# Kernel optimization log

Measured on AMD Instinct MI355X. Metric: run time of the kernel, lower is better.

## Reference

```python
import jax, jax.numpy as jnp
import numpy as np

B, DEC, ENC, H = 4, 128, 512, 768


def setup_inputs() -> dict:
    key = jax.random.key(0)
    k1, k2, k3, k4, k5 = jax.random.split(key, 5)
    scale = 1.0 / np.sqrt(H)
    return {
        "decoder_state": jax.random.normal(k1, (B, DEC, H), dtype=jnp.float32),
        "encoder_outputs": jax.random.normal(k2, (B, ENC, H), dtype=jnp.float32),
        "mask": jnp.zeros((B, DEC, ENC), dtype=jnp.float32),
        # Learned params: torch nn.Linear(H, H, bias=False) weights, stored as (in, out)
        "W1": jax.random.normal(k3, (H, H), dtype=jnp.float32) * scale,
        "W2": jax.random.normal(k4, (H, H), dtype=jnp.float32) * scale,
        "vt": jax.random.normal(k5, (H,), dtype=jnp.float32) * scale,
    }


def reference(decoder_state, encoder_outputs, mask, W1, W2, vt):
    # enc_t: (B, enc, H), dec_t: (B, dec, H)
    enc_t = jnp.einsum("beh,hk->bek", encoder_outputs, W1)
    dec_t = jnp.einsum("bdh,hk->bdk", decoder_state, W2)
    # Bahdanau additive score: tanh of broadcast sum -> (B, dec, enc, H), reduce with vt
    hidden = jnp.tanh(enc_t[:, None, :, :] + dec_t[:, :, None, :])
    log_score = jnp.einsum("bdek,k->bde", hidden, vt)
    log_score_masked = log_score + mask
    return (log_score_masked, log_score)
```

## Files before the change

### kernel.cpp

```cpp
#include <hip/hip_runtime.h>
#include <hip/hip_bf16.h>

#define B_SZ   4
#define DEC_SZ 128
#define ENC_SZ 512
#define H_SZ   768

typedef __attribute__((ext_vector_type(8))) short s8v;
typedef __attribute__((ext_vector_type(4))) float fvec4;

__device__ inline unsigned short f2bf(float x) {
  union { float f; unsigned u; } v; v.f = x;
  unsigned r = v.u + 0x7FFF + ((v.u >> 16) & 1);
  return (unsigned short)(r >> 16);
}

__global__ __launch_bounds__(256) void transpose_w(const float* __restrict__ W1,
                                                   const float* __restrict__ W2,
                                                   unsigned short* __restrict__ T1,
                                                   unsigned short* __restrict__ T2) {
  const float* W = blockIdx.z ? W2 : W1;
  unsigned short* T = blockIdx.z ? T2 : T1;
  __shared__ float tile[64][65];
  int c0 = blockIdx.x * 64;
  int r0 = blockIdx.y * 64;
  int tx = threadIdx.x & 63, ty = threadIdx.x >> 6;
#pragma unroll
  for (int i = 0; i < 16; ++i) {
    int r = ty + i * 4;
    tile[r][tx] = W[(size_t)(r0 + r) * H_SZ + c0 + tx];
  }
  __syncthreads();
#pragma unroll
  for (int i = 0; i < 16; ++i) {
    int c = ty + i * 4;
    T[(size_t)(c0 + c) * H_SZ + r0 + tx] = f2bf(tile[tx][c]);
  }
}

__global__ __launch_bounds__(256) void cast_bf16(const float* __restrict__ x,
                                                 unsigned short* __restrict__ y, int n4) {
  int i = blockIdx.x * 256 + threadIdx.x;
  if (i >= n4) return;
  float4 v = ((const float4*)x)[i];
  ushort4 o;
  o.x = f2bf(v.x); o.y = f2bf(v.y); o.z = f2bf(v.z); o.w = f2bf(v.w);
  ((ushort4*)y)[i] = o;
}

__global__ __launch_bounds__(256) void gemm_nt_exp(const unsigned short* __restrict__ A,
                                                   size_t strideA,
                                                   const unsigned short* __restrict__ Bm,
                                                   size_t strideB,
                                                   float* __restrict__ C, size_t strideC,
                                                   int ldc) {
  const int b  = blockIdx.z;
  const int m0 = blockIdx.x * 128;
  const int n0 = blockIdx.y * 128;
  const unsigned short* Ab = A + strideA * (size_t)b;
  const unsigned short* Bb = Bm + strideB * (size_t)b;

  __shared__ unsigned short As[128][40];
  __shared__ unsigned short Bs[128][40];

  const int tid  = threadIdx.x;
  const int wave = tid >> 6;
  const int lane = tid & 63;
  const int l16  = lane & 15;
  const int quad = lane >> 4;
  const int wm = (wave & 1) * 64;
  const int wn = (wave >> 1) * 64;

  fvec4 acc[4][4];
#pragma unroll
  for (int i = 0; i < 4; ++i)
#pragma unroll
    for (int j = 0; j < 4; ++j) acc[i][j] = (fvec4)0.f;

  for (int k0 = 0; k0 < H_SZ; k0 += 32) {
#pragma unroll
    for (int i = 0; i < 2; ++i) {
      int seg = tid + 256 * i;
      int r = seg >> 2, k8 = (seg & 3) * 8;
      *(s8v*)&As[r][k8] = *(const s8v*)(Ab + (size_t)(m0 + r) * H_SZ + k0 + k8);
      *(s8v*)&Bs[r][k8] = *(const s8v*)(Bb + (size_t)(n0 + r) * H_SZ + k0 + k8);
    }
    __syncthreads();

    s8v af[4], bf[4];
#pragma unroll
    for (int i = 0; i < 4; ++i) af[i] = *(const s8v*)&As[wm + i * 16 + l16][quad * 8];
#pragma unroll
    for (int j = 0; j < 4; ++j) bf[j] = *(const s8v*)&Bs[wn + j * 16 + l16][quad * 8];
#pragma unroll
    for (int i = 0; i < 4; ++i)
#pragma unroll
      for (int j = 0; j < 4; ++j)
        acc[i][j] = __builtin_amdgcn_mfma_f32_16x16x32_bf16(af[i], bf[j], acc[i][j], 0, 0, 0);
    __syncthreads();
  }

  const float C2 = 2.885390082f;
  float* Cb = C + strideC * (size_t)b;
#pragma unroll
  for (int i = 0; i < 4; ++i) {
    int m = m0 + wm + i * 16 + quad * 4;
#pragma unroll
    for (int j = 0; j < 4; ++j) {
      int n = n0 + wn + j * 16 + l16;
#pragma unroll
      for (int r = 0; r < 4; ++r)
        Cb[(size_t)(m + r) * ldc + n] = exp2f(acc[i][j][r] * C2);
    }
  }
}

#define D_CHUNK 8
#define K_CHUNK 96
#define NKC     8

__global__ __launch_bounds__(256) void score_kernel(const float* __restrict__ peT,
                                                    const float* __restrict__ pdm,
                                                    const float* __restrict__ vt,
                                                    float* __restrict__ part) {
  const int e  = blockIdx.x * 256 + threadIdx.x;
  const int d0 = blockIdx.y * D_CHUNK;
  const int bz = blockIdx.z;
  const int b  = bz >> 3;
  const int kc = bz & 7;
  const int k0 = kc * K_CHUNK;
  const int tid = threadIdx.x;

  __shared__ float pd_s[K_CHUNK][D_CHUNK];
  __shared__ float vts[K_CHUNK];

#pragma unroll
  for (int i = 0; i < 3; ++i) {
    int idx = tid + 256 * i;
    int d = idx / K_CHUNK, k = idx % K_CHUNK;
    pd_s[k][d] = pdm[((size_t)b * DEC_SZ + d0 + d) * H_SZ + k0 + k];
  }
  if (tid < K_CHUNK) vts[tid] = vt[k0 + tid];
  __syncthreads();

  float sumv = 0.f;
  for (int k = 0; k < K_CHUNK; ++k) sumv += vts[k];

  float t[D_CHUNK];
#pragma unroll
  for (int d = 0; d < D_CHUNK; ++d) t[d] = 0.f;

  const float* ep = peT + ((size_t)b * H_SZ + k0) * ENC_SZ + e;

#pragma unroll 4
  for (int k = 0; k < K_CHUNK; ++k) {
    float pe = ep[(size_t)k * ENC_SZ];
    float vk = vts[k];
    const float4 p0 = *(const float4*)&pd_s[k][0];
    const float4 p1 = *(const float4*)&pd_s[k][4];
    float pd[8] = {p0.x, p0.y, p0.z, p0.w, p1.x, p1.y, p1.z, p1.w};
#pragma unroll
    for (int d = 0; d < D_CHUNK; ++d) {
      float r = __builtin_amdgcn_rcpf(fmaf(pe, pd[d], 1.f));
      t[d] = fmaf(vk, r, t[d]);
    }
  }

  float* pp = part + (size_t)kc * (B_SZ * DEC_SZ * ENC_SZ) +
              ((size_t)b * DEC_SZ + d0) * ENC_SZ + e;
#pragma unroll
  for (int d = 0; d < D_CHUNK; ++d)
    pp[(size_t)d * ENC_SZ] = fmaf(-2.f, t[d], sumv);
}

__global__ __launch_bounds__(256) void finalize_kernel(const float* __restrict__ part,
                                                       const float* __restrict__ mask,
                                                       float* __restrict__ out) {
  const int N  = B_SZ * DEC_SZ * ENC_SZ;
  const int N4 = N / 4;
  int i = blockIdx.x * 256 + threadIdx.x;
  if (i >= N4) return;
  const float4* p = (const float4*)part;
  float4 s = p[i];
#pragma unroll
  for (int kc = 1; kc < NKC; ++kc) {
    float4 q = p[i + kc * N4];
    s.x += q.x; s.y += q.y; s.z += q.z; s.w += q.w;
  }
  float4 m = ((const float4*)mask)[i];
  float4 sm;
  sm.x = s.x + m.x; sm.y = s.y + m.y; sm.z = s.z + m.z; sm.w = s.w + m.w;
  ((float4*)out)[i] = sm;
  ((float4*)(out + N))[i] = s;
}

extern "C" void kernel_launch(void* const* d_in, const int* in_sizes, int n_in,
                              void* d_out, int out_size, void* d_ws, size_t ws_size,
                              hipStream_t stream) {
  (void)in_sizes; (void)n_in; (void)out_size; (void)ws_size;
  const float* dec  = (const float*)d_in[0];
  const float* enc  = (const float*)d_in[1];
  const float* mask = (const float*)d_in[2];
  const float* W1   = (const float*)d_in[3];
  const float* W2   = (const float*)d_in[4];
  const float* vt   = (const float*)d_in[5];
  float* out = (float*)d_out;

  float* peT  = (float*)d_ws;
  float* pdm  = peT + (size_t)B_SZ * H_SZ * ENC_SZ;
  float* part = pdm + (size_t)B_SZ * DEC_SZ * H_SZ;
  unsigned short* W1T  = (unsigned short*)(part + (size_t)NKC * B_SZ * DEC_SZ * ENC_SZ);
  unsigned short* W2T  = W1T + (size_t)H_SZ * H_SZ;
  unsigned short* encB = W2T + (size_t)H_SZ * H_SZ;
  unsigned short* decB = encB + (size_t)B_SZ * ENC_SZ * H_SZ;

  transpose_w<<<dim3(12, 12, 2), 256, 0, stream>>>(W1, W2, W1T, W2T);
  cast_bf16<<<dim3((B_SZ * ENC_SZ * H_SZ / 4 + 255) / 256), 256, 0, stream>>>(
      enc, encB, B_SZ * ENC_SZ * H_SZ / 4);
  cast_bf16<<<dim3((B_SZ * DEC_SZ * H_SZ / 4 + 255) / 256), 256, 0, stream>>>(
      dec, decB, B_SZ * DEC_SZ * H_SZ / 4);

  gemm_nt_exp<<<dim3(H_SZ / 128, ENC_SZ / 128, B_SZ), 256, 0, stream>>>(
      W1T, 0, encB, (size_t)ENC_SZ * H_SZ, peT, (size_t)H_SZ * ENC_SZ, ENC_SZ);
  gemm_nt_exp<<<dim3(DEC_SZ / 128, H_SZ / 128, B_SZ), 256, 0, stream>>>(
      decB, (size_t)DEC_SZ * H_SZ, W2T, 0, pdm, (size_t)DEC_SZ * H_SZ, H_SZ);

  score_kernel<<<dim3(ENC_SZ / 256, DEC_SZ / D_CHUNK, B_SZ * NKC), 256, 0, stream>>>(
      peT, pdm, vt, part);
  finalize_kernel<<<dim3(B_SZ * DEC_SZ * ENC_SZ / 4 / 256), 256, 0, stream>>>(
      part, mask, out);
}
```

Before: 145.7 us.

## Fuse score reduction with finalize, retile GEMMs with register prefetch, merge casts

Drops the split-K score kernel, its partial buffer and the separate finalize pass. A single score_out kernel now loops over all of H per (e, d) tile and writes both outputs with the mask added directly. The GEMMs switch to smaller templated tiles (TM x 64) with register prefetch of the next K slice, and batches fold into the M/N dimension. The two cast launches merge into one, and exp2f becomes the hardware builtin. This removes the partial-sum traffic and two launches, at the cost of less parallelism per score block (128 threads, full-K serial loop).

```diff
diff --git a/kernel.cpp b/kernel.cpp
--- a/kernel.cpp
+++ b/kernel.cpp
@@ -5,6 +5,7 @@
 #define DEC_SZ 128
 #define ENC_SZ 512
 #define H_SZ   768
+#define OUT_N  (B_SZ * DEC_SZ * ENC_SZ)
 
 typedef __attribute__((ext_vector_type(8))) short s8v;
 typedef __attribute__((ext_vector_type(4))) float fvec4;
@@ -38,8 +39,13 @@
   }
 }
 
-__global__ __launch_bounds__(256) void cast_bf16(const float* __restrict__ x,
-                                                 unsigned short* __restrict__ y, int n4) {
+__global__ __launch_bounds__(256) void cast_bf16(const float* __restrict__ enc,
+                                                 const float* __restrict__ dec,
+                                                 unsigned short* __restrict__ encB,
+                                                 unsigned short* __restrict__ decB) {
+  const float* x = blockIdx.z ? dec : enc;
+  unsigned short* y = blockIdx.z ? decB : encB;
+  int n4 = blockIdx.z ? (B_SZ * DEC_SZ * H_SZ / 4) : (B_SZ * ENC_SZ * H_SZ / 4);
   int i = blockIdx.x * 256 + threadIdx.x;
   if (i >= n4) return;
   float4 v = ((const float4*)x)[i];
@@ -48,150 +54,157 @@
   ((ushort4*)y)[i] = o;
 }
 
+template <int TM>
 __global__ __launch_bounds__(256) void gemm_nt_exp(const unsigned short* __restrict__ A,
-                                                   size_t strideA,
                                                    const unsigned short* __restrict__ Bm,
-                                                   size_t strideB,
-                                                   float* __restrict__ C, size_t strideC,
-                                                   int ldc) {
-  const int b  = blockIdx.z;
-  const int m0 = blockIdx.x * 128;
-  const int n0 = blockIdx.y * 128;
-  const unsigned short* Ab = A + strideA * (size_t)b;
-  const unsigned short* Bb = Bm + strideB * (size_t)b;
-
-  __shared__ unsigned short As[128][40];
-  __shared__ unsigned short Bs[128][40];
+                                                   float* __restrict__ C, int ldc) {
+  const int m0 = blockIdx.x * TM;
+  const int n0 = blockIdx.y * 64;
+
+  __shared__ unsigned short As[TM][40];
+  __shared__ unsigned short Bs[64][40];
 
   const int tid  = threadIdx.x;
   const int wave = tid >> 6;
   const int lane = tid & 63;
   const int l16  = lane & 15;
   const int quad = lane >> 4;
-  const int wm = (wave & 1) * 64;
-  const int wn = (wave >> 1) * 64;
-
-  fvec4 acc[4][4];
-#pragma unroll
-  for (int i = 0; i < 4; ++i)
+  const int MI   = TM / 64;
+  const int wm   = wave * (TM / 4);
+
+  const int ASEG = TM * 4 / 256;
+  int ar[2], ak[2];
+#pragma unroll
+  for (int i = 0; i < ASEG; ++i) {
+    int seg = tid + 256 * i;
+    ar[i] = seg >> 2; ak[i] = (seg & 3) * 8;
+  }
+  const int br = tid >> 2, bk = (tid & 3) * 8;
+
+  fvec4 acc[2][4];
+#pragma unroll
+  for (int i = 0; i < 2; ++i)
 #pragma unroll
     for (int j = 0; j < 4; ++j) acc[i][j] = (fvec4)0.f;
 
+  s8v pa[2], pb;
+#pragma unroll
+  for (int i = 0; i < ASEG; ++i)
+    pa[i] = *(const s8v*)(A + (size_t)(m0 + ar[i]) * H_SZ + ak[i]);
+  pb = *(const s8v*)(Bm + (size_t)(n0 + br) * H_SZ + bk);
+
   for (int k0 = 0; k0 < H_SZ; k0 += 32) {
-#pragma unroll
-    for (int i = 0; i < 2; ++i) {
-      int seg = tid + 256 * i;
-      int r = seg >> 2, k8 = (seg & 3) * 8;
-      *(s8v*)&As[r][k8] = *(const s8v*)(Ab + (size_t)(m0 + r) * H_SZ + k0 + k8);
-      *(s8v*)&Bs[r][k8] = *(const s8v*)(Bb + (size_t)(n0 + r) * H_SZ + k0 + k8);
-    }
     __syncthreads();
-
-    s8v af[4], bf[4];
-#pragma unroll
-    for (int i = 0; i < 4; ++i) af[i] = *(const s8v*)&As[wm + i * 16 + l16][quad * 8];
-#pragma unroll
-    for (int j = 0; j < 4; ++j) bf[j] = *(const s8v*)&Bs[wn + j * 16 + l16][quad * 8];
-#pragma unroll
-    for (int i = 0; i < 4; ++i)
+#pragma unroll
+    for (int i = 0; i < ASEG; ++i) *(s8v*)&As[ar[i]][ak[i]] = pa[i];
+    *(s8v*)&Bs[br][bk] = pb;
+    __syncthreads();
+
+    if (k0 + 32 < H_SZ) {
+#pragma unroll
+      for (int i = 0; i < ASEG; ++i)
+        pa[i] = *(const s8v*)(A + (size_t)(m0 + ar[i]) * H_SZ + k0 + 32 + ak[i]);
+      pb = *(const s8v*)(Bm + (size_t)(n0 + br) * H_SZ + k0 + 32 + bk);
+    }
+
+    s8v af[2], bf[4];
+#pragma unroll
+    for (int i = 0; i < MI; ++i) af[i] = *(const s8v*)&As[wm + i * 16 + l16][quad * 8];
+#pragma unroll
+    for (int j = 0; j < 4; ++j) bf[j] = *(const s8v*)&Bs[j * 16 + l16][quad * 8];
+#pragma unroll
+    for (int i = 0; i < MI; ++i)
 #pragma unroll
       for (int j = 0; j < 4; ++j)
         acc[i][j] = __builtin_amdgcn_mfma_f32_16x16x32_bf16(af[i], bf[j], acc[i][j], 0, 0, 0);
-    __syncthreads();
   }
 
   const float C2 = 2.885390082f;
-  float* Cb = C + strideC * (size_t)b;
-#pragma unroll
-  for (int i = 0; i < 4; ++i) {
+#pragma unroll
+  for (int i = 0; i < MI; ++i) {
     int m = m0 + wm + i * 16 + quad * 4;
 #pragma unroll
     for (int j = 0; j < 4; ++j) {
-      int n = n0 + wn + j * 16 + l16;
+      int n = n0 + j * 16 + l16;
 #pragma unroll
       for (int r = 0; r < 4; ++r)
-        Cb[(size_t)(m + r) * ldc + n] = exp2f(acc[i][j][r] * C2);
-    }
-  }
-}
-
-#define D_CHUNK 8
-#define K_CHUNK 96
-#define NKC     8
-
-__global__ __launch_bounds__(256) void score_kernel(const float* __restrict__ peT,
-                                                    const float* __restrict__ pdm,
-                                                    const float* __restrict__ vt,
-                                                    float* __restrict__ part) {
-  const int e  = blockIdx.x * 256 + threadIdx.x;
-  const int d0 = blockIdx.y * D_CHUNK;
-  const int bz = blockIdx.z;
-  const int b  = bz >> 3;
-  const int kc = bz & 7;
-  const int k0 = kc * K_CHUNK;
-  const int tid = threadIdx.x;
-
-  __shared__ float pd_s[K_CHUNK][D_CHUNK];
-  __shared__ float vts[K_CHUNK];
-
-#pragma unroll
-  for (int i = 0; i < 3; ++i) {
-    int idx = tid + 256 * i;
-    int d = idx / K_CHUNK, k = idx % K_CHUNK;
-    pd_s[k][d] = pdm[((size_t)b * DEC_SZ + d0 + d) * H_SZ + k0 + k];
-  }
-  if (tid < K_CHUNK) vts[tid] = vt[k0 + tid];
+        C[(size_t)(m + r) * ldc + n] = __builtin_amdgcn_exp2f(acc[i][j][r] * C2);
+    }
+  }
+}
+
+__global__ __launch_bounds__(128) void score_out(const float* __restrict__ peT,
+                                                 const float* __restrict__ pdm,
+                                                 const float* __restrict__ vt,
+                                                 const float* __restrict__ mask,
+                                                 float* __restrict__ out) {
+  const int tid  = threadIdx.x;
+  const int wave = tid >> 6;
+  const int lane = tid & 63;
+  const int e    = blockIdx.x * 64 + lane;
+  const int d0   = blockIdx.y * 8;
+  const int b    = blockIdx.z;
+
+  __shared__ float pd_s[H_SZ][8];
+  __shared__ float vts[H_SZ];
+
+  {
+    const int dloc = tid >> 4, l16 = tid & 15;
+    const float* row = pdm + (size_t)(b * DEC_SZ + d0 + dloc) * H_SZ;
+#pragma unroll
+    for (int i = 0; i < 12; ++i) {
+      int kb = (i * 16 + l16) * 4;
+      float4 v = *(const float4*)(row + kb);
+      pd_s[kb + 0][dloc] = v.x; pd_s[kb + 1][dloc] = v.y;
+      pd_s[kb + 2][dloc] = v.z; pd_s[kb + 3][dloc] = v.w;
+    }
+#pragma unroll
+    for (int i = 0; i < 6; ++i) vts[tid + 128 * i] = vt[tid + 128 * i];
+  }
   __syncthreads();
 
   float sumv = 0.f;
-  for (int k = 0; k < K_CHUNK; ++k) sumv += vts[k];
-
-  float t[D_CHUNK];
-#pragma unroll
-  for (int d = 0; d < D_CHUNK; ++d) t[d] = 0.f;
-
-  const float* ep = peT + ((size_t)b * H_SZ + k0) * ENC_SZ + e;
-
-#pragma unroll 4
-  for (int k = 0; k < K_CHUNK; ++k) {
-    float pe = ep[(size_t)k * ENC_SZ];
-    float vk = vts[k];
-    const float4 p0 = *(const float4*)&pd_s[k][0];
-    const float4 p1 = *(const float4*)&pd_s[k][4];
-    float pd[8] = {p0.x, p0.y, p0.z, p0.w, p1.x, p1.y, p1.z, p1.w};
-#pragma unroll
-    for (int d = 0; d < D_CHUNK; ++d) {
-      float r = __builtin_amdgcn_rcpf(fmaf(pe, pd[d], 1.f));
-      t[d] = fmaf(vk, r, t[d]);
-    }
-  }
-
-  float* pp = part + (size_t)kc * (B_SZ * DEC_SZ * ENC_SZ) +
-              ((size_t)b * DEC_SZ + d0) * ENC_SZ + e;
-#pragma unroll
-  for (int d = 0; d < D_CHUNK; ++d)
-    pp[(size_t)d * ENC_SZ] = fmaf(-2.f, t[d], sumv);
-}
-
-__global__ __launch_bounds__(256) void finalize_kernel(const float* __restrict__ part,
-                                                       const float* __restrict__ mask,
-                                                       float* __restrict__ out) {
-  const int N  = B_SZ * DEC_SZ * ENC_SZ;
-  const int N4 = N / 4;
-  int i = blockIdx.x * 256 + threadIdx.x;
-  if (i >= N4) return;
-  const float4* p = (const float4*)part;
-  float4 s = p[i];
-#pragma unroll
-  for (int kc = 1; kc < NKC; ++kc) {
-    float4 q = p[i + kc * N4];
-    s.x += q.x; s.y += q.y; s.z += q.z; s.w += q.w;
-  }
-  float4 m = ((const float4*)mask)[i];
-  float4 sm;
-  sm.x = s.x + m.x; sm.y = s.y + m.y; sm.z = s.z + m.z; sm.w = s.w + m.w;
-  ((float4*)out)[i] = sm;
-  ((float4*)(out + N))[i] = s;
+#pragma unroll
+  for (int j = 0; j < 12; ++j) sumv += vts[lane + 64 * j];
+#pragma unroll
+  for (int s = 1; s < 64; s <<= 1) sumv += __shfl_xor(sumv, s, 64);
+
+  float t[4] = {0.f, 0.f, 0.f, 0.f};
+  const float* pecol = peT + (size_t)b * ENC_SZ + e;
+
+  float buf[8];
+#pragma unroll
+  for (int i = 0; i < 8; ++i) buf[i] = pecol[(size_t)i * (B_SZ * ENC_SZ)];
+
+  for (int c = 0; c < H_SZ / 8; ++c) {
+    float cur[8];
+#pragma unroll
+    for (int i = 0; i < 8; ++i) cur[i] = buf[i];
+    if (c + 1 < H_SZ / 8) {
+#pragma unroll
+      for (int i = 0; i < 8; ++i)
+        buf[i] = pecol[(size_t)(c * 8 + 8 + i) * (B_SZ * ENC_SZ)];
+    }
+#pragma unroll
+    for (int i = 0; i < 8; ++i) {
+      int k = c * 8 + i;
+      float vk = vts[k];
+      const float4 pd4 = *(const float4*)&pd_s[k][wave * 4];
+      t[0] = fmaf(vk, __builtin_amdgcn_rcpf(fmaf(cur[i], pd4.x, 1.f)), t[0]);
+      t[1] = fmaf(vk, __builtin_amdgcn_rcpf(fmaf(cur[i], pd4.y, 1.f)), t[1]);
+      t[2] = fmaf(vk, __builtin_amdgcn_rcpf(fmaf(cur[i], pd4.z, 1.f)), t[2]);
+      t[3] = fmaf(vk, __builtin_amdgcn_rcpf(fmaf(cur[i], pd4.w, 1.f)), t[3]);
+    }
+  }
+
+#pragma unroll
+  for (int dd = 0; dd < 4; ++dd) {
+    int d = d0 + wave * 4 + dd;
+    size_t idx = ((size_t)(b * DEC_SZ + d)) * ENC_SZ + e;
+    float s = fmaf(-2.f, t[dd], sumv);
+    out[idx] = s + mask[idx];
+    out[OUT_N + idx] = s;
+  }
 }
 
 extern "C" void kernel_launch(void* const* d_in, const int* in_sizes, int n_in,
@@ -206,27 +219,22 @@
   const float* vt   = (const float*)d_in[5];
   float* out = (float*)d_out;
 
-  float* peT  = (float*)d_ws;
-  float* pdm  = peT + (size_t)B_SZ * H_SZ * ENC_SZ;
-  float* part = pdm + (size_t)B_SZ * DEC_SZ * H_SZ;
-  unsigned short* W1T  = (unsigned short*)(part + (size_t)NKC * B_SZ * DEC_SZ * ENC_SZ);
+  float* peT = (float*)d_ws;
+  float* pdm = peT + (size_t)H_SZ * B_SZ * ENC_SZ;
+  unsigned short* W1T  = (unsigned short*)(pdm + (size_t)B_SZ * DEC_SZ * H_SZ);
   unsigned short* W2T  = W1T + (size_t)H_SZ * H_SZ;
   unsigned short* encB = W2T + (size_t)H_SZ * H_SZ;
   unsigned short* decB = encB + (size_t)B_SZ * ENC_SZ * H_SZ;
 
   transpose_w<<<dim3(12, 12, 2), 256, 0, stream>>>(W1, W2, W1T, W2T);
-  cast_bf16<<<dim3((B_SZ * ENC_SZ * H_SZ / 4 + 255) / 256), 256, 0, stream>>>(
-      enc, encB, B_SZ * ENC_SZ * H_SZ / 4);
-  cast_bf16<<<dim3((B_SZ * DEC_SZ * H_SZ / 4 + 255) / 256), 256, 0, stream>>>(
-      dec, decB, B_SZ * DEC_SZ * H_SZ / 4);
-
-  gemm_nt_exp<<<dim3(H_SZ / 128, ENC_SZ / 128, B_SZ), 256, 0, stream>>>(
-      W1T, 0, encB, (size_t)ENC_SZ * H_SZ, peT, (size_t)H_SZ * ENC_SZ, ENC_SZ);
-  gemm_nt_exp<<<dim3(DEC_SZ / 128, H_SZ / 128, B_SZ), 256, 0, stream>>>(
-      decB, (size_t)DEC_SZ * H_SZ, W2T, 0, pdm, (size_t)DEC_SZ * H_SZ, H_SZ);
-
-  score_kernel<<<dim3(ENC_SZ / 256, DEC_SZ / D_CHUNK, B_SZ * NKC), 256, 0, stream>>>(
-      peT, pdm, vt, part);
-  finalize_kernel<<<dim3(B_SZ * DEC_SZ * ENC_SZ / 4 / 256), 256, 0, stream>>>(
-      part, mask, out);
-}
+  cast_bf16<<<dim3(B_SZ * ENC_SZ * H_SZ / 4 / 256, 1, 2), 256, 0, stream>>>(
+      enc, dec, encB, decB);
+
+  gemm_nt_exp<128><<<dim3(H_SZ / 128, B_SZ * ENC_SZ / 64), 256, 0, stream>>>(
+      W1T, encB, peT, B_SZ * ENC_SZ);
+  gemm_nt_exp<64><<<dim3(B_SZ * DEC_SZ / 64, H_SZ / 64), 256, 0, stream>>>(
+      decB, W2T, pdm, H_SZ);
+
+  score_out<<<dim3(ENC_SZ / 64, DEC_SZ / 8, B_SZ), 128, 0, stream>>>(
+      peT, pdm, vt, mask, out);
+}
```

New measurement: 154.6 us. 1.06x slower.
